# Kernel tuning notes

Measured on AMD Instinct MI355X. Metric: run time of the kernel, lower is better.

Reference implementation:

```python
import jax, jax.numpy as jnp
import numpy as np

RES_MIN, RES_MAX, L, S_DIM = 16, 256, 16, 512
T = 65536           # hash table entries per level (power of 2)
B = 8
N = RES_MAX * RES_MAX
PRIME = np.uint32(2654435761)


def _res_levels():
    # Instant-NGP geometric progression of grid resolutions.
    b = (RES_MAX / RES_MIN) ** (1.0 / (L - 1))
    r = np.round(RES_MIN * b ** np.arange(L)).astype(np.int64)
    return np.minimum(r, RES_MAX)

RES_LEVELS = _res_levels()


def _sample_coords():
    # row-major grid, coord = (x, y) normalized to (0,1), index n = y*R + x
    yy, xx = np.meshgrid(np.arange(RES_MAX), np.arange(RES_MAX), indexing='ij')
    c = np.stack([(xx + 0.5) / RES_MAX, (yy + 0.5) / RES_MAX], axis=-1)
    return c.reshape(-1, 2).astype(np.float32)  # [N, 2]


def hash_retrieve(tables, coords):
    # tables: [B, L, T, 2], coords: [N, 2] in (0,1) -> [B, N, L*2]
    res_f = jnp.asarray(RES_LEVELS, jnp.float32)[:, None, None]          # [L,1,1]
    pos = coords[None, :, :] * (res_f - 1.0)                              # [L,N,2]
    pos0 = jnp.floor(pos)
    frac = pos - pos0                                                     # [L,N,2]
    i0 = pos0.astype(jnp.uint32)
    imax = (jnp.asarray(RES_LEVELS, jnp.uint32) - 1)[:, None, None]
    i1 = jnp.minimum(i0 + 1, imax)
    x0, y0 = i0[..., 0], i0[..., 1]
    x1, y1 = i1[..., 0], i1[..., 1]

    def hsh(xi, yi):  # spatial hash mod table size
        return ((xi ^ (yi * PRIME)) % np.uint32(T)).astype(jnp.int32)

    idx = jnp.stack([hsh(x0, y0), hsh(x1, y0), hsh(x0, y1), hsh(x1, y1)], -1)  # [L,N,4]
    tab = jnp.transpose(tables, (1, 0, 2, 3))                             # [L,B,T,2]
    # per-level gather: [L,B,N,4,2]
    g = jax.vmap(lambda t, i: t[:, i], in_axes=(0, 0))(tab, idx)
    fx, fy = frac[..., 0], frac[..., 1]
    w = jnp.stack([(1 - fx) * (1 - fy), fx * (1 - fy), (1 - fx) * fy, fx * fy], -1)  # [L,N,4]
    feats = jnp.sum(g * w[:, None, :, :, None], axis=3)                   # [L,B,N,2]
    feats = jnp.transpose(feats, (1, 2, 0, 3))                            # [B,N,L,2]
    return feats.reshape(feats.shape[0], feats.shape[1], L * 2)


def mod_linear(xin, s, w, aw, ab, bias, activ):
    # StyleGAN2 modulated linear with demodulation.
    style = s @ aw.T + ab                                 # [B, in]
    wmod = w[None, :, :] * style[:, None, :]              # [B, out, in]
    demod = jax.lax.rsqrt(jnp.sum(wmod * wmod, -1) + 1e-8)  # [B, out]
    y = jnp.einsum('bni,boi->bno', xin, wmod) * demod[:, None, :] + bias
    return activ(y)


def setup_inputs() -> dict:
    key = jax.random.key(0)
    ks = jax.random.split(key, 16)
    d = {
        'x': jax.random.normal(ks[0], (B, L, T * 2), jnp.float32),
        's': jax.random.normal(ks[1], (B, S_DIM), jnp.float32),
        'coords': jnp.asarray(_sample_coords()),
    }
    dims = [(L * 2, 32), (32, 32), (32, 3)]
    for i, (cin, cout) in enumerate(dims):
        d[f'w{i}'] = jax.random.normal(ks[2 + 4 * i], (cout, cin), jnp.float32) / np.sqrt(cin)
        d[f'aw{i}'] = jax.random.normal(ks[3 + 4 * i], (cin, S_DIM), jnp.float32) / np.sqrt(S_DIM)
        d[f'ab{i}'] = jnp.ones((cin,), jnp.float32)
        d[f'b{i}'] = jnp.zeros((cout,), jnp.float32)
    return d


def reference(x, s, coords, w0, aw0, ab0, b0, w1, aw1, ab1, b1, w2, aw2, ab2, b2):
    tables = x.reshape(B, L, T, 2)
    h = hash_retrieve(tables, coords)                      # [B, N, 32]
    h = mod_linear(h, s, w0, aw0, ab0, b0, jax.nn.relu)
    h = mod_linear(h, s, w1, aw1, ab1, b1, jax.nn.relu)
    h = mod_linear(h, s, w2, aw2, ab2, b2, jnp.tanh)       # [B, N, 3]
    img = h.reshape(B, RES_MAX, RES_MAX, 3)
    return jnp.transpose(img, (0, 3, 1, 2))                # [B,3,H,W]
```

## Files before the change

kernel.cpp:

```cpp
#include <hip/hip_runtime.h>
#include <math.h>

#define LVL 16
#define TBL 65536
#define BATCH 8
#define NPIX 65536
#define SDIM 512
#define HPRIME 2654435761u

typedef __attribute__((ext_vector_type(2))) float f32x2;

struct ResPack { int r[LVL]; };
struct OffPack { int o[LVL]; };

#define WEFF_STRIDE 2144

__global__ __launch_bounds__(256) void weff_kernel(
    const float* __restrict__ s,
    const float* __restrict__ aw0, const float* __restrict__ ab0,
    const float* __restrict__ aw1, const float* __restrict__ ab1,
    const float* __restrict__ aw2, const float* __restrict__ ab2,
    const float* __restrict__ w0, const float* __restrict__ w1,
    const float* __restrict__ w2,
    float* __restrict__ ws)
{
    const int b = blockIdx.x & 7;
    const int l = blockIdx.x >> 3;
    const int tid = (int)threadIdx.x;
    const int wave = tid >> 6, lane = tid & 63;

    const float* aw; const float* ab; const float* w; int nout;
    if (l == 0)      { aw = aw0; ab = ab0; w = w0; nout = 32; }
    else if (l == 1) { aw = aw1; ab = ab1; w = w1; nout = 32; }
    else             { aw = aw2; ab = ab2; w = w2; nout = 3;  }

    __shared__ float st[32];
    __shared__ float dem[32];

    const float* sb = s + b * SDIM;
    for (int r0 = wave * 8; r0 < wave * 8 + 8; r0 += 2) {
        const float* rowA = aw + (size_t)r0 * SDIM;
        const float* rowB = aw + (size_t)(r0 + 1) * SDIM;
        float a0 = 0.f, a1 = 0.f;
        #pragma unroll
        for (int j = 0; j < SDIM / 64; ++j) {
            const int k = lane + j * 64;
            const float sv = sb[k];
            a0 += sv * rowA[k];
            a1 += sv * rowB[k];
        }
        #pragma unroll
        for (int off = 32; off >= 1; off >>= 1) {
            a0 += __shfl_xor(a0, off, 64);
            a1 += __shfl_xor(a1, off, 64);
        }
        if (lane == 0) { st[r0] = a0 + ab[r0]; st[r0 + 1] = a1 + ab[r0 + 1]; }
    }
    __syncthreads();

    {
        const int o = tid >> 3, sub = tid & 7;
        if (o < nout) {
            float sum = 0.f;
            #pragma unroll
            for (int j = 0; j < 4; ++j) {
                const int i = sub * 4 + j;
                const float v = w[o * 32 + i] * st[i];
                sum += v * v;
            }
            sum += __shfl_xor(sum, 4, 64);
            sum += __shfl_xor(sum, 2, 64);
            sum += __shfl_xor(sum, 1, 64);
            if (sub == 0) dem[o] = 1.0f / sqrtf(sum + 1e-8f);
        }
    }
    __syncthreads();

    float* outp = ws + (size_t)b * WEFF_STRIDE;
    if (l < 2) {
        const int base = l * 1024;
        for (int idx = tid; idx < 1024; idx += 256) {
            const int o2 = idx >> 6, rem = idx & 63, i = rem >> 1, h = rem & 1;
            const int oo = o2 + 16 * h;
            outp[base + idx] = w[oo * 32 + i] * st[i] * dem[oo];
        }
    } else {
        if (tid < 96) {
            const int oo = tid >> 5, i = tid & 31;
            outp[2048 + tid] = w[tid] * st[i] * dem[oo];
        }
    }
}

__global__ __launch_bounds__(256) void fused_kernel(
    const float* __restrict__ tables,
    const float* __restrict__ coords,
    const float* __restrict__ weff,
    const float* __restrict__ b0, const float* __restrict__ b1, const float* __restrict__ b2,
    float* __restrict__ out,
    ResPack rp, OffPack op)
{
    const int b     = blockIdx.x & 7;
    const int chunk = blockIdx.x >> 3;
    const int tid   = (int)threadIdx.x;
    const int n     = chunk * 256 + tid;

    __shared__ float2 blend[1600];

    const float* tb = tables + (size_t)b * (LVL * TBL * 2);

    const float cy = coords[(chunk << 9) + 1];

    #pragma unroll
    for (int l = 0; l < LVL; ++l) {
        const int R = rp.r[l];
        if (tid < R) {
            const float rm1 = (float)(R - 1);
            const float py  = cy * rm1;
            const float fpy = floorf(py);
            const float fy  = py - fpy;
            int y0 = (int)fpy;
            int y1 = y0 + 1; if (y1 > R - 1) y1 = R - 1;
            const unsigned hy0 = (unsigned)y0 * HPRIME;
            const unsigned hy1 = (unsigned)y1 * HPRIME;
            const unsigned x   = (unsigned)tid;
            const unsigned h0  = (x ^ hy0) & 0xFFFFu;
            const unsigned h1  = (x ^ hy1) & 0xFFFFu;
            const float2* tl = (const float2*)tb + (size_t)l * TBL;
            const float2 g0 = tl[h0];
            const float2 g1 = tl[h1];
            float2 r;
            r.x = g0.x * (1.f - fy) + g1.x * fy;
            r.y = g0.y * (1.f - fy) + g1.y * fy;
            blend[op.o[l] + tid] = r;
        }
    }
    __syncthreads();

    const float cx = coords[2 * n];
    float feat[32];
    #pragma unroll
    for (int l = 0; l < LVL; ++l) {
        const int R = rp.r[l];
        const float rm1 = (float)(R - 1);
        const float px  = cx * rm1;
        const float fpx = floorf(px);
        const float fx  = px - fpx;
        int x0 = (int)fpx;
        int x1 = x0 + 1; if (x1 > R - 1) x1 = R - 1;
        const int base = op.o[l];
        const float2 gA = blend[base + x0];
        const float2 gB = blend[base + x1];
        feat[2 * l]     = gA.x * (1.f - fx) + gB.x * fx;
        feat[2 * l + 1] = gA.y * (1.f - fx) + gB.y * fx;
    }

    const f32x2* W0p = (const f32x2*)(weff + (size_t)b * WEFF_STRIDE);
    const f32x2* W1p = W0p + 512;
    const float* W2  = weff + (size_t)b * WEFF_STRIDE + 2048;

    f32x2 h1p[16];
    #pragma unroll
    for (int o2 = 0; o2 < 16; ++o2) {
        f32x2 acc; acc[0] = b0[o2]; acc[1] = b0[o2 + 16];
        #pragma unroll
        for (int i = 0; i < 32; ++i) {
            f32x2 fb; fb[0] = feat[i]; fb[1] = feat[i];
            acc += W0p[o2 * 32 + i] * fb;
        }
        acc[0] = fmaxf(acc[0], 0.f); acc[1] = fmaxf(acc[1], 0.f);
        h1p[o2] = acc;
    }

    f32x2 h2p[16];
    #pragma unroll
    for (int o2 = 0; o2 < 16; ++o2) {
        f32x2 acc; acc[0] = b1[o2]; acc[1] = b1[o2 + 16];
        #pragma unroll
        for (int i = 0; i < 32; ++i) {
            const float hv = h1p[i & 15][i >> 4];
            f32x2 fb; fb[0] = hv; fb[1] = hv;
            acc += W1p[o2 * 32 + i] * fb;
        }
        acc[0] = fmaxf(acc[0], 0.f); acc[1] = fmaxf(acc[1], 0.f);
        h2p[o2] = acc;
    }

    #pragma unroll
    for (int o = 0; o < 3; ++o) {
        float acc = b2[o];
        #pragma unroll
        for (int i = 0; i < 32; ++i)
            acc = fmaf(W2[o * 32 + i], h2p[i & 15][i >> 4], acc);
        out[((size_t)(b * 3 + o) << 16) + n] = tanhf(acc);
    }
}

extern "C" void kernel_launch(void* const* d_in, const int* in_sizes, int n_in,
                              void* d_out, int out_size, void* d_ws, size_t ws_size,
                              hipStream_t stream) {
    const float* x      = (const float*)d_in[0];
    const float* s      = (const float*)d_in[1];
    const float* coords = (const float*)d_in[2];
    const float* w0  = (const float*)d_in[3];
    const float* aw0 = (const float*)d_in[4];
    const float* ab0 = (const float*)d_in[5];
    const float* b0  = (const float*)d_in[6];
    const float* w1  = (const float*)d_in[7];
    const float* aw1 = (const float*)d_in[8];
    const float* ab1 = (const float*)d_in[9];
    const float* b1  = (const float*)d_in[10];
    const float* w2  = (const float*)d_in[11];
    const float* aw2 = (const float*)d_in[12];
    const float* ab2 = (const float*)d_in[13];
    const float* b2  = (const float*)d_in[14];
    float* out = (float*)d_out;
    float* ws  = (float*)d_ws;

    ResPack rp; OffPack op;
    const double g = pow(256.0 / 16.0, 1.0 / 15.0);
    int cum = 0;
    for (int l = 0; l < LVL; ++l) {
        double r = 16.0 * pow(g, (double)l);
        long ri = lround(r);
        if (ri > 256) ri = 256;
        rp.r[l] = (int)ri;
        op.o[l] = cum;
        cum += (int)ri;
    }

    hipLaunchKernelGGL(weff_kernel, dim3(24), dim3(256), 0, stream,
                       s, aw0, ab0, aw1, ab1, aw2, ab2, w0, w1, w2, ws);
    hipLaunchKernelGGL(fused_kernel, dim3(NPIX / 256 * BATCH), dim3(256), 0, stream,
                       x, coords, ws, b0, b1, b2, out, rp, op);
}
```

Measured before the change: 175.4 us.

## Process four rows per block with double-buffered row blend prefetch

Each block now handles four image rows instead of one. The next row's hash-table gathers are issued before the current row's MLP runs, and their blends are written into a second shared buffer afterwards. A precomputed level/x plan lets all 256 threads share the fill work evenly, where before only threads below each level's resolution did it. The goal is to hide gather latency behind MLP compute and cut idle threads in the fill phase. In exchange the grid is four times smaller (512 blocks), registers are held across the MLP, and shared memory per block grows.

```diff
diff --git a/kernel.cpp b/kernel.cpp
--- a/kernel.cpp
+++ b/kernel.cpp
@@ -8,12 +8,17 @@
 #define SDIM 512
 #define HPRIME 2654435761u
 
+#define NROWS 4
+#define MAXCUM 1472
+#define FITERS 6
+
 typedef __attribute__((ext_vector_type(2))) float f32x2;
 
 struct ResPack { int r[LVL]; };
 struct OffPack { int o[LVL]; };
 
 #define WEFF_STRIDE 2144
+#define PLAN_OFF    17152
 
 __global__ __launch_bounds__(256) void weff_kernel(
     const float* __restrict__ s,
@@ -22,12 +27,24 @@
     const float* __restrict__ aw2, const float* __restrict__ ab2,
     const float* __restrict__ w0, const float* __restrict__ w1,
     const float* __restrict__ w2,
-    float* __restrict__ ws)
+    float* __restrict__ ws, OffPack op, int cum)
 {
     const int b = blockIdx.x & 7;
     const int l = blockIdx.x >> 3;
     const int tid = (int)threadIdx.x;
     const int wave = tid >> 6, lane = tid & 63;
+
+    if (blockIdx.x == 0) {
+        unsigned short* plan = (unsigned short*)(ws + PLAN_OFF);
+        for (int i = tid; i < cum; i += 256) {
+            int lv = 0, base = 0;
+            #pragma unroll
+            for (int t = 1; t < LVL; ++t) {
+                if (i >= op.o[t]) { lv = t; base = op.o[t]; }
+            }
+            plan[i] = (unsigned short)((lv << 8) | (i - base));
+        }
+    }
 
     const float* aw; const float* ab; const float* w; int nout;
     if (l == 0)      { aw = aw0; ab = ab0; w = w0; nout = 32; }
@@ -96,104 +113,160 @@
     const float* __restrict__ tables,
     const float* __restrict__ coords,
     const float* __restrict__ weff,
+    const unsigned short* __restrict__ plan,
     const float* __restrict__ b0, const float* __restrict__ b1, const float* __restrict__ b2,
     float* __restrict__ out,
-    ResPack rp, OffPack op)
+    ResPack rp, OffPack op, int cum)
 {
-    const int b     = blockIdx.x & 7;
-    const int chunk = blockIdx.x >> 3;
-    const int tid   = (int)threadIdx.x;
-    const int n     = chunk * 256 + tid;
-
-    __shared__ float2 blend[1600];
-
-    const float* tb = tables + (size_t)b * (LVL * TBL * 2);
-
-    const float cy = coords[(chunk << 9) + 1];
-
+    const int b    = blockIdx.x & 7;
+    const int grp  = blockIdx.x >> 3;
+    const int tid  = (int)threadIdx.x;
+    const int row0 = grp * NROWS;
+
+    __shared__ float2 blend[2][MAXCUM];
+    __shared__ float rm1t[LVL];
+
+    const float2* tb2 = (const float2*)tables + (size_t)b * (LVL * TBL);
+
+    if (tid == 0) {
+        #pragma unroll
+        for (int l = 0; l < LVL; ++l) rm1t[l] = (float)(rp.r[l] - 1);
+    }
+    unsigned short pe[FITERS];
     #pragma unroll
-    for (int l = 0; l < LVL; ++l) {
-        const int R = rp.r[l];
-        if (tid < R) {
-            const float rm1 = (float)(R - 1);
-            const float py  = cy * rm1;
-            const float fpy = floorf(py);
-            const float fy  = py - fpy;
-            int y0 = (int)fpy;
-            int y1 = y0 + 1; if (y1 > R - 1) y1 = R - 1;
-            const unsigned hy0 = (unsigned)y0 * HPRIME;
-            const unsigned hy1 = (unsigned)y1 * HPRIME;
-            const unsigned x   = (unsigned)tid;
-            const unsigned h0  = (x ^ hy0) & 0xFFFFu;
-            const unsigned h1  = (x ^ hy1) & 0xFFFFu;
-            const float2* tl = (const float2*)tb + (size_t)l * TBL;
-            const float2 g0 = tl[h0];
-            const float2 g1 = tl[h1];
-            float2 r;
-            r.x = g0.x * (1.f - fy) + g1.x * fy;
-            r.y = g0.y * (1.f - fy) + g1.y * fy;
-            blend[op.o[l] + tid] = r;
-        }
+    for (int k = 0; k < FITERS; ++k) {
+        const int i = k * 256 + tid;
+        pe[k] = (i < cum) ? plan[i] : (unsigned short)0;
+    }
+    float cyv[NROWS], cxv[NROWS];
+    #pragma unroll
+    for (int r = 0; r < NROWS; ++r) {
+        cyv[r] = coords[((row0 + r) << 9) + 1];
+        cxv[r] = coords[((row0 + r) << 9) + 2 * tid];
     }
     __syncthreads();
 
-    const float cx = coords[2 * n];
-    float feat[32];
+    int lvv[FITERS], xxv[FITERS];
+    float rm1v[FITERS];
     #pragma unroll
-    for (int l = 0; l < LVL; ++l) {
-        const int R = rp.r[l];
-        const float rm1 = (float)(R - 1);
-        const float px  = cx * rm1;
-        const float fpx = floorf(px);
-        const float fx  = px - fpx;
-        int x0 = (int)fpx;
-        int x1 = x0 + 1; if (x1 > R - 1) x1 = R - 1;
-        const int base = op.o[l];
-        const float2 gA = blend[base + x0];
-        const float2 gB = blend[base + x1];
-        feat[2 * l]     = gA.x * (1.f - fx) + gB.x * fx;
-        feat[2 * l + 1] = gA.y * (1.f - fx) + gB.y * fx;
-    }
+    for (int k = 0; k < FITERS; ++k) {
+        lvv[k]  = pe[k] >> 8;
+        xxv[k]  = pe[k] & 255;
+        rm1v[k] = rm1t[lvv[k]];
+    }
+
+    float2 g0v[FITERS], g1v[FITERS];
+    float  fyv[FITERS];
+
+#define FILL_ISSUE(CY) do {                                                    \
+    _Pragma("unroll")                                                          \
+    for (int k = 0; k < FITERS; ++k) {                                         \
+        const float rm1 = rm1v[k];                                             \
+        const float py  = (CY) * rm1;                                          \
+        const float fpy = floorf(py);                                          \
+        fyv[k] = py - fpy;                                                     \
+        int y0 = (int)fpy;                                                     \
+        int y1 = y0 + 1; const int ym = (int)rm1; if (y1 > ym) y1 = ym;        \
+        const unsigned h0 = ((unsigned)xxv[k] ^ ((unsigned)y0 * HPRIME)) & 0xFFFFu; \
+        const unsigned h1 = ((unsigned)xxv[k] ^ ((unsigned)y1 * HPRIME)) & 0xFFFFu; \
+        const int base = lvv[k] << 16;                                         \
+        if (k * 256 + tid < cum) {                                             \
+            g0v[k] = tb2[base + (int)h0];                                      \
+            g1v[k] = tb2[base + (int)h1];                                      \
+        }                                                                      \
+    }                                                                          \
+} while (0)
+
+#define FILL_WRITE(BUF) do {                                                   \
+    _Pragma("unroll")                                                          \
+    for (int k = 0; k < FITERS; ++k) {                                         \
+        const int i = k * 256 + tid;                                           \
+        if (i < cum) {                                                         \
+            const float fy = fyv[k]; const float ofy = 1.f - fy;               \
+            float2 rr;                                                         \
+            rr.x = g0v[k].x * ofy + g1v[k].x * fy;                             \
+            rr.y = g0v[k].y * ofy + g1v[k].y * fy;                             \
+            blend[BUF][i] = rr;                                                \
+        }                                                                      \
+    }                                                                          \
+} while (0)
+
+    FILL_ISSUE(cyv[0]);
+    FILL_WRITE(0);
+    __syncthreads();
 
     const f32x2* W0p = (const f32x2*)(weff + (size_t)b * WEFF_STRIDE);
     const f32x2* W1p = W0p + 512;
     const float* W2  = weff + (size_t)b * WEFF_STRIDE + 2048;
 
-    f32x2 h1p[16];
     #pragma unroll
-    for (int o2 = 0; o2 < 16; ++o2) {
-        f32x2 acc; acc[0] = b0[o2]; acc[1] = b0[o2 + 16];
-        #pragma unroll
-        for (int i = 0; i < 32; ++i) {
-            f32x2 fb; fb[0] = feat[i]; fb[1] = feat[i];
-            acc += W0p[o2 * 32 + i] * fb;
-        }
-        acc[0] = fmaxf(acc[0], 0.f); acc[1] = fmaxf(acc[1], 0.f);
-        h1p[o2] = acc;
-    }
-
-    f32x2 h2p[16];
-    #pragma unroll
-    for (int o2 = 0; o2 < 16; ++o2) {
-        f32x2 acc; acc[0] = b1[o2]; acc[1] = b1[o2 + 16];
-        #pragma unroll
-        for (int i = 0; i < 32; ++i) {
-            const float hv = h1p[i & 15][i >> 4];
-            f32x2 fb; fb[0] = hv; fb[1] = hv;
-            acc += W1p[o2 * 32 + i] * fb;
-        }
-        acc[0] = fmaxf(acc[0], 0.f); acc[1] = fmaxf(acc[1], 0.f);
-        h2p[o2] = acc;
-    }
-
-    #pragma unroll
-    for (int o = 0; o < 3; ++o) {
-        float acc = b2[o];
-        #pragma unroll
-        for (int i = 0; i < 32; ++i)
-            acc = fmaf(W2[o * 32 + i], h2p[i & 15][i >> 4], acc);
-        out[((size_t)(b * 3 + o) << 16) + n] = tanhf(acc);
-    }
+    for (int r = 0; r < NROWS; ++r) {
+        const int cur = r & 1;
+
+        if (r + 1 < NROWS) FILL_ISSUE(cyv[r + 1]);
+
+        const float2* bp = blend[cur];
+        const float cx = cxv[r];
+        float feat[32];
+        #pragma unroll
+        for (int l = 0; l < LVL; ++l) {
+            const int R = rp.r[l];
+            const float rm1 = (float)(R - 1);
+            const float px  = cx * rm1;
+            const float fpx = floorf(px);
+            const float fx  = px - fpx;
+            int x0 = (int)fpx;
+            int x1 = x0 + 1; if (x1 > R - 1) x1 = R - 1;
+            const int base = op.o[l];
+            const float2 gA = bp[base + x0];
+            const float2 gB = bp[base + x1];
+            const float ofx = 1.f - fx;
+            feat[2 * l]     = gA.x * ofx + gB.x * fx;
+            feat[2 * l + 1] = gA.y * ofx + gB.y * fx;
+        }
+
+        f32x2 h1p[16];
+        #pragma unroll
+        for (int o2 = 0; o2 < 16; ++o2) {
+            f32x2 acc; acc[0] = b0[o2]; acc[1] = b0[o2 + 16];
+            #pragma unroll
+            for (int i = 0; i < 32; ++i) {
+                f32x2 fb; fb[0] = feat[i]; fb[1] = feat[i];
+                acc += W0p[o2 * 32 + i] * fb;
+            }
+            acc[0] = fmaxf(acc[0], 0.f); acc[1] = fmaxf(acc[1], 0.f);
+            h1p[o2] = acc;
+        }
+
+        f32x2 h2p[16];
+        #pragma unroll
+        for (int o2 = 0; o2 < 16; ++o2) {
+            f32x2 acc; acc[0] = b1[o2]; acc[1] = b1[o2 + 16];
+            #pragma unroll
+            for (int i = 0; i < 32; ++i) {
+                const float hv = h1p[i & 15][i >> 4];
+                f32x2 fb; fb[0] = hv; fb[1] = hv;
+                acc += W1p[o2 * 32 + i] * fb;
+            }
+            acc[0] = fmaxf(acc[0], 0.f); acc[1] = fmaxf(acc[1], 0.f);
+            h2p[o2] = acc;
+        }
+
+        const int n = (row0 + r) * 256 + tid;
+        #pragma unroll
+        for (int o = 0; o < 3; ++o) {
+            float acc = b2[o];
+            #pragma unroll
+            for (int i = 0; i < 32; ++i)
+                acc = fmaf(W2[o * 32 + i], h2p[i & 15][i >> 4], acc);
+            out[((size_t)(b * 3 + o) << 16) + n] = tanhf(acc);
+        }
+
+        if (r + 1 < NROWS) FILL_WRITE(cur ^ 1);
+        __syncthreads();
+    }
+#undef FILL_ISSUE
+#undef FILL_WRITE
 }
 
 extern "C" void kernel_launch(void* const* d_in, const int* in_sizes, int n_in,
@@ -230,7 +303,9 @@
     }
 
     hipLaunchKernelGGL(weff_kernel, dim3(24), dim3(256), 0, stream,
-                       s, aw0, ab0, aw1, ab1, aw2, ab2, w0, w1, w2, ws);
-    hipLaunchKernelGGL(fused_kernel, dim3(NPIX / 256 * BATCH), dim3(256), 0, stream,
-                       x, coords, ws, b0, b1, b2, out, rp, op);
+                       s, aw0, ab0, aw1, ab1, aw2, ab2, w0, w1, w2, ws, op, cum);
+    hipLaunchKernelGGL(fused_kernel, dim3((256 / NROWS) * BATCH), dim3(256), 0, stream,
+                       x, coords, ws,
+                       (const unsigned short*)(ws + PLAN_OFF),
+                       b0, b1, b2, out, rp, op, cum);
 }
```

Result: slower. 186.2 us (+6.2%).
